# Performance work log

Hardware: AMD Instinct MI355X
Metric: run time of the kernel (lower is better)

## Reference

```python
import jax, jax.numpy as jnp
import numpy as np

N_NODES = 8192
D_FEAT = 128
R_BITS = 8      # rows per band
B_BANDS = 64    # number of LSH bands
D_THRESH = 0.25 # cosine-distance threshold from LSH(z, d=0.25, ...)


def setup_inputs() -> dict:
    key = jax.random.key(0)
    k1, k2, k3 = jax.random.split(key, 3)
    z = jax.random.normal(k1, (N_NODES, D_FEAT), dtype=jnp.float32)
    # random hyperplanes for signed-projection LSH: r*b = 512 planes
    H = jax.random.normal(k2, (D_FEAT, R_BITS * B_BANDS), dtype=jnp.float32)
    edge_index = jax.random.randint(k3, (2, N_NODES * 16), 0, N_NODES, dtype=jnp.int64)
    return {"z": z, "H": H, "edge_index": edge_index}


def reference(z, H, edge_index):
    # edge_index is unused by forward_all (kept for signature fidelity).
    N = z.shape[0]
    # --- hyperplane LSH signatures ---
    bits = (z @ H) > 0                              # [N, r*b] bool
    bits = bits.reshape(N, B_BANDS, R_BITS)         # [N, b, r]
    powers = (2 ** jnp.arange(R_BITS)).astype(jnp.int32)
    codes = jnp.sum(bits.astype(jnp.int32) * powers, axis=-1)  # [N, b] band hash codes

    # --- candidate pairs: collide in at least one band (OR over bands) ---
    def band_or(mask, c):  # c: [N] codes for one band
        return mask | (c[:, None] == c[None, :]), None
    collide, _ = jax.lax.scan(band_or, jnp.zeros((N, N), dtype=bool), codes.T)

    # --- exact cosine similarity on candidates ---
    zn = z / jnp.linalg.norm(z, axis=1, keepdims=True)
    S = zn @ zn.T                                   # [N, N] cosine similarity
    dist = 1.0 - S                                  # cosine distance

    eye = jnp.eye(N, dtype=bool)
    # pairs kept by LSH: colliding, within distance threshold, off-diagonal
    keep = collide & (dist < D_THRESH) & (~eye)
    # adjacency[v1, v2] = 1 - dist = cos_sim (sigmoid=True path); identity on diagonal
    A = jnp.where(keep, S, 0.0) + eye.astype(S.dtype)
    return A
```

## Files before the change

### kernel.cpp

```cpp
#include <hip/hip_runtime.h>
#include <hip/hip_bf16.h>

#define N_NODES 8192
#define D_FEAT 128
#define NWORDS 8

typedef __bf16 bf16x8 __attribute__((ext_vector_type(8)));
typedef float f32x4 __attribute__((ext_vector_type(4)));
typedef unsigned long long u64;

__global__ __launch_bounds__(512, 4) void prep_kernel(const float* __restrict__ z,
                                                      const float* __restrict__ H,
                                                      unsigned short* __restrict__ zn,
                                                      u64* __restrict__ codes) {
  int tid = threadIdx.x;
  int base = blockIdx.x * 16;

  {
    int n = tid >> 5, sub = tid & 31;
    const float4* row = (const float4*)(z + (size_t)(base + n) * D_FEAT);
    float4 v = row[sub];
    float ss = v.x * v.x + v.y * v.y + v.z * v.z + v.w * v.w;
#pragma unroll
    for (int off = 16; off > 0; off >>= 1) ss += __shfl_xor(ss, off);
    float inv = rsqrtf(ss);
    __hip_bfloat16 b0 = __float2bfloat16(v.x * inv);
    __hip_bfloat16 b1 = __float2bfloat16(v.y * inv);
    __hip_bfloat16 b2 = __float2bfloat16(v.z * inv);
    __hip_bfloat16 b3 = __float2bfloat16(v.w * inv);
    ushort4 o;
    o.x = *(unsigned short*)&b0; o.y = *(unsigned short*)&b1;
    o.z = *(unsigned short*)&b2; o.w = *(unsigned short*)&b3;
    *(ushort4*)&zn[(size_t)(base + n) * D_FEAT + sub * 4] = o;
  }

  int w = tid >> 6, lane = tid & 63;
  int col = w * 64 + lane;
  const float4* z4 = (const float4*)z;

  float acc[16];
#pragma unroll
  for (int n = 0; n < 16; ++n) acc[n] = 0.f;

  for (int k4 = 0; k4 < 32; ++k4) {
    float4 h;
    h.x = H[(size_t)(k4 * 4 + 0) * 512 + col];
    h.y = H[(size_t)(k4 * 4 + 1) * 512 + col];
    h.z = H[(size_t)(k4 * 4 + 2) * 512 + col];
    h.w = H[(size_t)(k4 * 4 + 3) * 512 + col];
    float4 zv[16];
#pragma unroll
    for (int n = 0; n < 16; ++n) zv[n] = z4[(size_t)(base + n) * 32 + k4];
#pragma unroll
    for (int n = 0; n < 16; ++n)
      acc[n] += zv[n].x * h.x + zv[n].y * h.y + zv[n].z * h.z + zv[n].w * h.w;
  }

#pragma unroll
  for (int n = 0; n < 16; ++n) {
    u64 b = __ballot(acc[n] > 0.0f);
    if (lane == 0) codes[(size_t)(base + n) * NWORDS + w] = b;
  }
}

__global__ __launch_bounds__(256, 2) void sim_kernel(const unsigned short* __restrict__ zn,
                                                     const u64* __restrict__ codes,
                                                     float* __restrict__ out) {
  __shared__ __align__(16) unsigned char smem_raw[65536];
  unsigned short (*As)[128] = (unsigned short (*)[128])smem_raw;
  unsigned short (*Bs)[128] = (unsigned short (*)[128])(smem_raw + 32768);
  float* fS = (float*)smem_raw;

  int tid = threadIdx.x;
  int bm = blockIdx.x, bn = blockIdx.y;

  const uint4* gA = (const uint4*)(zn + (size_t)bm * 128 * D_FEAT);
  const uint4* gB = (const uint4*)(zn + (size_t)bn * 128 * D_FEAT);
#pragma unroll
  for (int r = 0; r < 8; ++r) {
    int idx = tid + 256 * r;
    int row = idx >> 4, c16 = idx & 15;
    int cs = c16 ^ (row & 15);
    ((uint4*)&As[row][0])[cs] = gA[idx];
    ((uint4*)&Bs[row][0])[cs] = gB[idx];
  }
  __syncthreads();

  int wv = tid >> 6, lane = tid & 63;
  int wm = (wv >> 1) * 64, wn = (wv & 1) * 64;
  int m16 = lane & 15, g = lane >> 4;

  f32x4 acc[4][4] = {};

#pragma unroll
  for (int kc = 0; kc < 4; ++kc) {
    bf16x8 fa[4], fb[4];
    int chunk = kc * 4 + g;
    int cs = (chunk ^ m16) * 8;
#pragma unroll
    for (int t = 0; t < 4; ++t) {
      fa[t] = *(const bf16x8*)&As[wm + t * 16 + m16][cs];
      fb[t] = *(const bf16x8*)&Bs[wn + t * 16 + m16][cs];
    }
#pragma unroll
    for (int tm = 0; tm < 4; ++tm)
#pragma unroll
      for (int tn = 0; tn < 4; ++tn)
        acc[tm][tn] = __builtin_amdgcn_mfma_f32_16x16x32_bf16(fa[tm], fb[tn], acc[tm][tn], 0, 0, 0);
  }

  __syncthreads();

#pragma unroll
  for (int tm = 0; tm < 4; ++tm) {
#pragma unroll
    for (int tn = 0; tn < 4; ++tn) {
      int col = wn + tn * 16 + m16;
      int j = bn * 128 + col;
      f32x4 c = acc[tm][tn];
#pragma unroll
      for (int r = 0; r < 4; ++r) {
        int row = wm + tm * 16 + g * 4 + r;
        int i = bm * 128 + row;
        float s = c[r];
        float val = 0.0f;
        if (i == j) {
          val = 1.0f;
        } else if (s > 0.75f) {
          bool hit = false;
#pragma unroll
          for (int w = 0; w < NWORDS; ++w) {
            u64 x = codes[(size_t)i * NWORDS + w] ^ codes[(size_t)j * NWORDS + w];
            u64 hz = (x - 0x0101010101010101ULL) & ~x & 0x8080808080808080ULL;
            hit |= (hz != 0);
          }
          if (hit) val = s;
        }
        fS[row * 128 + ((((col >> 2) ^ (row & 31)) << 2) | (col & 3))] = val;
      }
    }
  }
  __syncthreads();

#pragma unroll
  for (int r = 0; r < 16; ++r) {
    int slot = tid + 256 * r;
    int row = slot >> 5, chunk = slot & 31;
    f32x4 v = *(const f32x4*)&fS[row * 128 + ((chunk ^ (row & 31)) << 2)];
    __builtin_nontemporal_store(
        v, (f32x4*)&out[(size_t)(bm * 128 + row) * N_NODES + bn * 128 + chunk * 4]);
  }
}

extern "C" void kernel_launch(void* const* d_in, const int* in_sizes, int n_in,
                              void* d_out, int out_size, void* d_ws, size_t ws_size,
                              hipStream_t stream) {
  const float* z = (const float*)d_in[0];
  const float* H = (const float*)d_in[1];
  float* out = (float*)d_out;

  unsigned short* zn = (unsigned short*)d_ws;
  u64* codes = (u64*)((char*)d_ws + (size_t)N_NODES * D_FEAT * 2);

  prep_kernel<<<N_NODES / 16, 512, 0, stream>>>(z, H, zn, codes);
  sim_kernel<<<dim3(64, 64), 256, 0, stream>>>(zn, codes, out);
}
```

Measured before the change: 318.7 us.

## Fuse normalization and LSH into similarity kernel, compute band codes lazily

Removes the separate prep kernel. Each similarity block now normalizes its z rows and converts them to bf16 itself. LSH band collisions are checked by recomputing hyperplane projections only for pairs that pass the cosine threshold, and the output store switches from nontemporal to a plain store. This saves one launch and the workspace traffic, at the cost of redundant normalization per tile and a very slow per-pair LSH path if many pairs pass the threshold.

New measurement: 300.6 us. -5.7%, faster.

```diff
diff --git a/kernel.cpp b/kernel.cpp
--- a/kernel.cpp
+++ b/kernel.cpp
@@ -3,68 +3,39 @@
 
 #define N_NODES 8192
 #define D_FEAT 128
-#define NWORDS 8
 
 typedef __bf16 bf16x8 __attribute__((ext_vector_type(8)));
 typedef float f32x4 __attribute__((ext_vector_type(4)));
 typedef unsigned long long u64;
 
-__global__ __launch_bounds__(512, 4) void prep_kernel(const float* __restrict__ z,
-                                                      const float* __restrict__ H,
-                                                      unsigned short* __restrict__ zn,
-                                                      u64* __restrict__ codes) {
-  int tid = threadIdx.x;
-  int base = blockIdx.x * 16;
-
-  {
-    int n = tid >> 5, sub = tid & 31;
-    const float4* row = (const float4*)(z + (size_t)(base + n) * D_FEAT);
-    float4 v = row[sub];
-    float ss = v.x * v.x + v.y * v.y + v.z * v.z + v.w * v.w;
-#pragma unroll
-    for (int off = 16; off > 0; off >>= 1) ss += __shfl_xor(ss, off);
-    float inv = rsqrtf(ss);
-    __hip_bfloat16 b0 = __float2bfloat16(v.x * inv);
-    __hip_bfloat16 b1 = __float2bfloat16(v.y * inv);
-    __hip_bfloat16 b2 = __float2bfloat16(v.z * inv);
-    __hip_bfloat16 b3 = __float2bfloat16(v.w * inv);
-    ushort4 o;
-    o.x = *(unsigned short*)&b0; o.y = *(unsigned short*)&b1;
-    o.z = *(unsigned short*)&b2; o.w = *(unsigned short*)&b3;
-    *(ushort4*)&zn[(size_t)(base + n) * D_FEAT + sub * 4] = o;
+__device__ __attribute__((noinline)) bool lsh_collide(
+    const float* __restrict__ z, const float* __restrict__ H, int i, int j) {
+  for (int b = 0; b < 64; ++b) {
+    unsigned ci = 0, cj = 0;
+    for (int bit = 0; bit < 8; ++bit) {
+      int col = b * 8 + bit;
+      float di = 0.f, dj = 0.f;
+      for (int k = 0; k < D_FEAT; ++k) {
+        float h = H[(size_t)k * 512 + col];
+        di += z[(size_t)i * D_FEAT + k] * h;
+        dj += z[(size_t)j * D_FEAT + k] * h;
+      }
+      if (di > 0.f) ci |= (1u << bit);
+      if (dj > 0.f) cj |= (1u << bit);
+    }
+    if (ci == cj) return true;
   }
-
-  int w = tid >> 6, lane = tid & 63;
-  int col = w * 64 + lane;
-  const float4* z4 = (const float4*)z;
-
-  float acc[16];
-#pragma unroll
-  for (int n = 0; n < 16; ++n) acc[n] = 0.f;
-
-  for (int k4 = 0; k4 < 32; ++k4) {
-    float4 h;
-    h.x = H[(size_t)(k4 * 4 + 0) * 512 + col];
-    h.y = H[(size_t)(k4 * 4 + 1) * 512 + col];
-    h.z = H[(size_t)(k4 * 4 + 2) * 512 + col];
-    h.w = H[(size_t)(k4 * 4 + 3) * 512 + col];
-    float4 zv[16];
-#pragma unroll
-    for (int n = 0; n < 16; ++n) zv[n] = z4[(size_t)(base + n) * 32 + k4];
-#pragma unroll
-    for (int n = 0; n < 16; ++n)
-      acc[n] += zv[n].x * h.x + zv[n].y * h.y + zv[n].z * h.z + zv[n].w * h.w;
-  }
-
-#pragma unroll
-  for (int n = 0; n < 16; ++n) {
-    u64 b = __ballot(acc[n] > 0.0f);
-    if (lane == 0) codes[(size_t)(base + n) * NWORDS + w] = b;
-  }
+  return false;
 }
 
-__global__ __launch_bounds__(256, 2) void sim_kernel(const unsigned short* __restrict__ zn,
-                                                     const u64* __restrict__ codes,
+__device__ __forceinline__ unsigned pack_bf16x2(float x, float y) {
+  __hip_bfloat16 bx = __float2bfloat16(x), by = __float2bfloat16(y);
+  return (unsigned)(*(unsigned short*)&bx) |
+         ((unsigned)(*(unsigned short*)&by) << 16);
+}
+
+__global__ __launch_bounds__(256, 2) void sim_kernel(const float* __restrict__ z,
+                                                     const float* __restrict__ H,
                                                      float* __restrict__ out) {
   __shared__ __align__(16) unsigned char smem_raw[65536];
   unsigned short (*As)[128] = (unsigned short (*)[128])smem_raw;
@@ -74,15 +45,34 @@
   int tid = threadIdx.x;
   int bm = blockIdx.x, bn = blockIdx.y;
 
-  const uint4* gA = (const uint4*)(zn + (size_t)bm * 128 * D_FEAT);
-  const uint4* gB = (const uint4*)(zn + (size_t)bn * 128 * D_FEAT);
+  {
+    int row = tid >> 1, half = tid & 1;
 #pragma unroll
-  for (int r = 0; r < 8; ++r) {
-    int idx = tid + 256 * r;
-    int row = idx >> 4, c16 = idx & 15;
-    int cs = c16 ^ (row & 15);
-    ((uint4*)&As[row][0])[cs] = gA[idx];
-    ((uint4*)&Bs[row][0])[cs] = gB[idx];
+    for (int pass = 0; pass < 2; ++pass) {
+      int gr = (pass ? bn : bm) * 128 + row;
+      const float4* src = (const float4*)(z + (size_t)gr * D_FEAT + half * 64);
+      float4 v[16];
+#pragma unroll
+      for (int c = 0; c < 16; ++c) v[c] = src[c];
+      float ss = 0.f;
+#pragma unroll
+      for (int c = 0; c < 16; ++c)
+        ss += v[c].x * v[c].x + v[c].y * v[c].y + v[c].z * v[c].z + v[c].w * v[c].w;
+      ss += __shfl_xor(ss, 1);
+      float inv = rsqrtf(ss);
+      unsigned short (*T)[128] = pass ? Bs : As;
+#pragma unroll
+      for (int c = 0; c < 8; ++c) {
+        float4 a = v[2 * c], b = v[2 * c + 1];
+        uint4 o;
+        o.x = pack_bf16x2(a.x * inv, a.y * inv);
+        o.y = pack_bf16x2(a.z * inv, a.w * inv);
+        o.z = pack_bf16x2(b.x * inv, b.y * inv);
+        o.w = pack_bf16x2(b.z * inv, b.w * inv);
+        int cg = half * 8 + c;
+        ((uint4*)&T[row][0])[cg ^ (row & 15)] = o;
+      }
+    }
   }
   __syncthreads();
 
@@ -127,14 +117,7 @@
         if (i == j) {
           val = 1.0f;
         } else if (s > 0.75f) {
-          bool hit = false;
-#pragma unroll
-          for (int w = 0; w < NWORDS; ++w) {
-            u64 x = codes[(size_t)i * NWORDS + w] ^ codes[(size_t)j * NWORDS + w];
-            u64 hz = (x - 0x0101010101010101ULL) & ~x & 0x8080808080808080ULL;
-            hit |= (hz != 0);
-          }
-          if (hit) val = s;
+          if (lsh_collide(z, H, i, j)) val = s;
         }
         fS[row * 128 + ((((col >> 2) ^ (row & 31)) << 2) | (col & 3))] = val;
       }
@@ -146,9 +129,8 @@
   for (int r = 0; r < 16; ++r) {
     int slot = tid + 256 * r;
     int row = slot >> 5, chunk = slot & 31;
-    f32x4 v = *(const f32x4*)&fS[row * 128 + ((chunk ^ (row & 31)) << 2)];
-    __builtin_nontemporal_store(
-        v, (f32x4*)&out[(size_t)(bm * 128 + row) * N_NODES + bn * 128 + chunk * 4]);
+    float4 v = *(const float4*)&fS[row * 128 + ((chunk ^ (row & 31)) << 2)];
+    *(float4*)&out[(size_t)(bm * 128 + row) * N_NODES + bn * 128 + chunk * 4] = v;
   }
 }
 
@@ -158,10 +140,7 @@
   const float* z = (const float*)d_in[0];
   const float* H = (const float*)d_in[1];
   float* out = (float*)d_out;
+  (void)d_ws; (void)ws_size;
 
-  unsigned short* zn = (unsigned short*)d_ws;
-  u64* codes = (u64*)((char*)d_ws + (size_t)N_NODES * D_FEAT * 2);
-
-  prep_kernel<<<N_NODES / 16, 512, 0, stream>>>(z, H, zn, codes);
-  sim_kernel<<<dim3(64, 64), 256, 0, stream>>>(zn, codes, out);
+  sim_kernel<<<dim3(64, 64), 256, 0, stream>>>(z, H, out);
 }
```
